# Performance work log

Measured on AMD Instinct MI355X. Metric: run time of the kernel, lower is better.

## Reference

```python
import jax, jax.numpy as jnp
import numpy as np

IN_F = 256
OUT_F = 256
ALPHA = 0.2  # leaky-relu slope
NEG_INF = -9e15


def setup_inputs() -> dict:
    key = jax.random.key(0)
    ks = jax.random.split(key, 8)
    N_e, N_kc = 10000, 2000
    exercise_h = jax.random.normal(ks[0], (N_e, IN_F), dtype=jnp.float32)
    kc_h = jax.random.normal(ks[1], (N_kc, IN_F), dtype=jnp.float32)
    adj = jax.random.randint(ks[2], (N_e, N_kc), 0, 2, dtype=jnp.int32)
    # parameters (kaiming-ish scaling)
    W1 = jax.random.normal(ks[3], (IN_F, OUT_F), dtype=jnp.float32) * np.sqrt(2.0 / IN_F)
    E = jax.random.normal(ks[4], (IN_F, OUT_F), dtype=jnp.float32) * np.sqrt(2.0 / IN_F)
    a = jax.random.normal(ks[5], (2 * OUT_F, 1), dtype=jnp.float32) * np.sqrt(2.0 / (2 * OUT_F))
    rd_w = jax.random.normal(ks[6], (OUT_F, 2 * OUT_F), dtype=jnp.float32) * np.sqrt(2.0 / (2 * OUT_F))
    rd_b = jnp.zeros((OUT_F,), dtype=jnp.float32)
    return {"exercise_h": exercise_h, "kc_h": kc_h, "adj": adj,
            "W1": W1, "E": E, "a": a, "rd_w": rd_w, "rd_b": rd_b}


def reference(exercise_h, kc_h, adj, W1, E, a, rd_w, rd_b):
    kc_Wh = kc_h @ W1            # [N_kc, D]
    ex_Wh = exercise_h @ W1      # [N_e, D]
    # a . concat(ex_Wh_i, kc_Wh_j) == a1.ex_Wh_i + a2.kc_Wh_j  (avoids [N_e,N_kc,2D] tensor)
    a1 = a[:OUT_F, 0]
    a2 = a[OUT_F:, 0]
    e = jax.nn.leaky_relu((ex_Wh @ a1)[:, None] + (kc_Wh @ a2)[None, :], negative_slope=ALPHA)  # [N_e, N_kc]
    logits = jnp.where(adj > 0, e, jnp.float32(NEG_INF))
    attention = jax.nn.softmax(logits, axis=1)
    new_kc = attention @ kc_Wh           # [N_e, D]
    ex_Eh = exercise_h @ E               # [N_e, D]
    feat = jnp.concatenate([new_kc, new_kc * ex_Eh], axis=1)  # [N_e, 2D]
    out = feat @ rd_w.T + rd_b
    return jax.nn.elu(out)
```

## Files before the change

### kernel.cpp

```cpp
#include <hip/hip_runtime.h>

#define N_E 10000
#define N_KC 2000
#define KPAD 2048
#define ALPHA 0.2f

typedef __attribute__((ext_vector_type(8))) short short8;
typedef __attribute__((ext_vector_type(4))) float f32x4;

__device__ float g_w1a1[256];
__device__ float g_w1a2[256];
__device__ float g_s[N_E];
__device__ float g_t[KPAD];
__device__ __align__(16) unsigned short g_kc_bf[N_KC * 256];
__device__ __align__(16) unsigned short g_exh_pk[625 * 8 * 512];
__device__ __align__(16) unsigned short g_W1T_pk[16 * 8 * 512];
__device__ __align__(16) unsigned short g_ET_pk[16 * 8 * 512];
__device__ __align__(16) unsigned short g_rdw_pk[16 * 16 * 512];
__device__ __align__(16) unsigned short g_kcWh_pk[16 * 64 * 512];

__device__ __forceinline__ unsigned short f2bf(float f) {
  union { float f; unsigned int u; } v; v.f = f;
  unsigned int r = v.u + 0x7FFFu + ((v.u >> 16) & 1u);
  return (unsigned short)(r >> 16);
}

__device__ __forceinline__ void cvt_store4(float4 v, unsigned short* dst) {
  ushort4 o;
  o.x = f2bf(v.x); o.y = f2bf(v.y); o.z = f2bf(v.z); o.w = f2bf(v.w);
  *reinterpret_cast<ushort4*>(dst) = o;
}

__global__ __launch_bounds__(256) void prep_kernel(
    const float* __restrict__ exh, const float* __restrict__ kc_h,
    const float* __restrict__ W1, const float* __restrict__ E,
    const float* __restrict__ a, const float* __restrict__ rd_w) {
  int b = blockIdx.x, tid = threadIdx.x;
  if (b < 625) {
#pragma unroll
    for (int s2 = 0; s2 < 2; ++s2) {
      int sId = tid + s2 * 256;
      int kt = sId >> 6, lane = sId & 63;
      int g = lane >> 4, r = lane & 15;
      const float* src = exh + (size_t)(b * 16 + r) * 256 + kt * 32 + g * 8;
      unsigned short* dst = g_exh_pk + ((size_t)b * 8 + kt) * 512 + lane * 8;
      cvt_store4(*(const float4*)src, dst);
      cvt_store4(*(const float4*)(src + 4), dst + 4);
    }
  } else if (b < 750) {
    for (int q = 0; q < 4; ++q) {
      int idx = (b - 625) * 1024 + q * 256 + tid;
      cvt_store4(((const float4*)kc_h)[idx], g_kc_bf + (size_t)idx * 4);
    }
  } else if (b < 782) {
#pragma unroll
    for (int s2 = 0; s2 < 2; ++s2) {
      int sId = (b - 750) * 512 + tid + s2 * 256;
      int ct = sId >> 10, rem = sId & 1023;
      int kt = rem >> 6, lane = rem & 63;
      int g = lane >> 4, r = lane & 15;
      const float* src = rd_w + (size_t)(ct * 16 + r) * 512 + kt * 32 + g * 8;
      unsigned short* dst = g_rdw_pk + (size_t)sId * 8;
      cvt_store4(*(const float4*)src, dst);
      cvt_store4(*(const float4*)(src + 4), dst + 4);
    }
  } else if (b < 798) {
#pragma unroll
    for (int s2 = 0; s2 < 2; ++s2) {
      int sId = (b - 782) * 512 + tid + s2 * 256;
      int ct = sId >> 9, rem = sId & 511;
      int kt = rem >> 6, lane = rem & 63;
      int g = lane >> 4, r = lane & 15;
      int col = ct * 16 + r, k = kt * 32 + g * 8;
      unsigned short* dst = g_W1T_pk + (size_t)sId * 8;
      ushort4 o0, o1;
      o0.x = f2bf(W1[(k + 0) * 256 + col]); o0.y = f2bf(W1[(k + 1) * 256 + col]);
      o0.z = f2bf(W1[(k + 2) * 256 + col]); o0.w = f2bf(W1[(k + 3) * 256 + col]);
      o1.x = f2bf(W1[(k + 4) * 256 + col]); o1.y = f2bf(W1[(k + 5) * 256 + col]);
      o1.z = f2bf(W1[(k + 6) * 256 + col]); o1.w = f2bf(W1[(k + 7) * 256 + col]);
      *(ushort4*)dst = o0; *(ushort4*)(dst + 4) = o1;
    }
  } else if (b < 814) {
#pragma unroll
    for (int s2 = 0; s2 < 2; ++s2) {
      int sId = (b - 798) * 512 + tid + s2 * 256;
      int ct = sId >> 9, rem = sId & 511;
      int kt = rem >> 6, lane = rem & 63;
      int g = lane >> 4, r = lane & 15;
      int col = ct * 16 + r, k = kt * 32 + g * 8;
      unsigned short* dst = g_ET_pk + (size_t)sId * 8;
      ushort4 o0, o1;
      o0.x = f2bf(E[(k + 0) * 256 + col]); o0.y = f2bf(E[(k + 1) * 256 + col]);
      o0.z = f2bf(E[(k + 2) * 256 + col]); o0.w = f2bf(E[(k + 3) * 256 + col]);
      o1.x = f2bf(E[(k + 4) * 256 + col]); o1.y = f2bf(E[(k + 5) * 256 + col]);
      o1.z = f2bf(E[(k + 6) * 256 + col]); o1.w = f2bf(E[(k + 7) * 256 + col]);
      *(ushort4*)dst = o0; *(ushort4*)(dst + 4) = o1;
    }
  } else if (b < 816) {
    const float* av = a + (b - 814) * 256;
    float acc = 0.f;
    for (int q = 0; q < 64; ++q) {
      float4 wv = *(const float4*)(W1 + (size_t)tid * 256 + q * 4);
      float4 a4 = *(const float4*)(av + q * 4);
      acc += wv.x * a4.x + wv.y * a4.y + wv.z * a4.z + wv.w * a4.w;
    }
    if (b == 814) g_w1a1[tid] = acc; else g_w1a2[tid] = acc;
  } else {
    for (int idx = tid; idx < 16 * 2 * 512; idx += 256) {
      int ct = idx >> 10, rem = idx & 1023;
      int kt = 62 + (rem >> 9), off = rem & 511;
      g_kcWh_pk[((size_t)ct * 64 + kt) * 512 + off] = 0;
    }
    if (tid < 48) g_t[2000 + tid] = 0.f;
  }
}

__global__ __launch_bounds__(256) void st_kernel(
    const float* __restrict__ exh, const float* __restrict__ kc_h) {
  int tid = threadIdx.x, lane = tid & 63, w = tid >> 6;
  int row = blockIdx.x * 4 + w;
  bool is_s = row < N_E;
  const float* src = is_s ? (exh + (size_t)row * 256)
                          : (kc_h + (size_t)(row - N_E) * 256);
  const float* wv = is_s ? g_w1a1 : g_w1a2;
  float4 x = *(const float4*)(src + lane * 4);
  float4 c = *(const float4*)(wv + lane * 4);
  float d = x.x * c.x + x.y * c.y + x.z * c.z + x.w * c.w;
  for (int off = 32; off; off >>= 1) d += __shfl_down(d, off, 64);
  if (lane == 0) { if (is_s) g_s[row] = d; else g_t[row - N_E] = d; }
}

__global__ __launch_bounds__(256) void kc_mfma_kernel() {
  int tid = threadIdx.x, lane = tid & 63, w = tid >> 6;
  int r = lane & 15, g = lane >> 4;
  int j0 = blockIdx.x * 16;
  f32x4 acc[4] = {{0.f,0.f,0.f,0.f},{0.f,0.f,0.f,0.f},
                  {0.f,0.f,0.f,0.f},{0.f,0.f,0.f,0.f}};
  for (int kk = 0; kk < 8; ++kk) {
    int k = kk * 32 + g * 8;
    short8 afrag = *(const short8*)(g_kc_bf + (size_t)(j0 + r) * 256 + k);
#pragma unroll
    for (int n = 0; n < 4; ++n) {
      short8 bfrag =
          *(const short8*)(g_W1T_pk + ((size_t)(w * 4 + n) * 8 + kk) * 512 +
                           lane * 8);
      acc[n] = __builtin_amdgcn_mfma_f32_16x16x32_bf16(afrag, bfrag, acc[n],
                                                       0, 0, 0);
    }
  }
  int j = j0 + g * 4;
  int kt = j >> 5, lsub = ((j >> 3) & 3) * 16 + r, sub = (g & 1) * 4;
#pragma unroll
  for (int n = 0; n < 4; ++n) {
    int ct = w * 4 + n;
    ushort4 o;
    o.x = f2bf(acc[n][0]); o.y = f2bf(acc[n][1]);
    o.z = f2bf(acc[n][2]); o.w = f2bf(acc[n][3]);
    *reinterpret_cast<ushort4*>(
        g_kcWh_pk + ((size_t)ct * 64 + kt) * 512 + lsub * 8 + sub) = o;
  }
}

#define PST 280
#define FST 536
__global__ __launch_bounds__(512) void main_kernel(
    const int* __restrict__ adj, const float* __restrict__ rd_b,
    float* __restrict__ out) {
  __shared__ float t_s[KPAD];
  __shared__ __align__(16) unsigned short p_s[2][16 * PST];
  __shared__ __align__(16) unsigned short feat_s[16 * FST];
  __shared__ float ds_part[8][16];
  __shared__ float dtot[16];

  int tid = threadIdx.x;
  int w = tid >> 6, lane = tid & 63;
  int r = lane & 15, g = lane >> 4;
  int i0 = blockIdx.x * 16;
  int c0e = w * 32;

  for (int q = tid; q < KPAD / 4; q += 512)
    ((float4*)t_s)[q] = ((const float4*)g_t)[q];
  float sv = g_s[i0 + r];
  const int* arow = adj + (size_t)(i0 + r) * N_KC;
  __syncthreads();

  f32x4 accP[2] = {{0.f,0.f,0.f,0.f},{0.f,0.f,0.f,0.f}};
  float dsum = 0.f;

  auto gen = [&](int c) {
    int kk = c * 8 + w;
    unsigned short* dst = &p_s[c & 1][r * PST + w * 32 + g * 8];
    int c0 = kk * 32 + g * 8;
    int4 pk = {0, 0, 0, 0};
    if (kk < 63 && c0 < N_KC) {
      int4 a0 = *(const int4*)(arow + c0);
      int4 a1 = *(const int4*)(arow + c0 + 4);
      float4 t0 = *(const float4*)(t_s + c0);
      float4 t1 = *(const float4*)(t_s + c0 + 4);
      float tv[8] = {t0.x, t0.y, t0.z, t0.w, t1.x, t1.y, t1.z, t1.w};
      int av[8] = {a0.x, a0.y, a0.z, a0.w, a1.x, a1.y, a1.z, a1.w};
      unsigned int ub[8];
#pragma unroll
      for (int j = 0; j < 8; ++j) {
        float x = sv + tv[j];
        float lx = fmaxf(x, ALPHA * x);
        float pv = (av[j] > 0) ? __expf(lx) : 0.f;
        dsum += pv;
        ub[j] = __float_as_uint(pv) + 0x8000u;
      }
      pk.x = (int)((ub[0] >> 16) | (ub[1] & 0xFFFF0000u));
      pk.y = (int)((ub[2] >> 16) | (ub[3] & 0xFFFF0000u));
      pk.z = (int)((ub[4] >> 16) | (ub[5] & 0xFFFF0000u));
      pk.w = (int)((ub[6] >> 16) | (ub[7] & 0xFFFF0000u));
    }
    *(int4*)dst = pk;
  };

  auto mfma_chunk = [&](int c) {
#pragma unroll
    for (int u = 0; u < 8; ++u) {
      int kk = c * 8 + u;
      short8 af = *(const short8*)&p_s[c & 1][r * PST + u * 32 + g * 8];
#pragma unroll
      for (int n = 0; n < 2; ++n) {
        short8 bf = *(const short8*)(g_kcWh_pk +
                                     ((size_t)(w * 2 + n) * 64 + kk) * 512 +
                                     lane * 8);
        accP[n] = __builtin_amdgcn_mfma_f32_16x16x32_bf16(af, bf, accP[n],
                                                          0, 0, 0);
      }
    }
  };

  gen(0);
  __syncthreads();
  for (int c = 1; c < 8; ++c) {
    gen(c);
    mfma_chunk(c - 1);
    __syncthreads();
  }
  mfma_chunk(7);

  dsum += __shfl_xor(dsum, 16, 64);
  dsum += __shfl_xor(dsum, 32, 64);
  if (lane < 16) ds_part[w][lane] = dsum;

  f32x4 accE[2] = {{0.f,0.f,0.f,0.f},{0.f,0.f,0.f,0.f}};
#pragma unroll
  for (int kk = 0; kk < 8; ++kk) {
    short8 af = *(const short8*)(g_exh_pk +
                                 ((size_t)blockIdx.x * 8 + kk) * 512 + lane * 8);
#pragma unroll
    for (int n = 0; n < 2; ++n) {
      short8 bf = *(const short8*)(g_ET_pk +
                                   ((size_t)(w * 2 + n) * 8 + kk) * 512 +
                                   lane * 8);
      accE[n] = __builtin_amdgcn_mfma_f32_16x16x32_bf16(af, bf, accE[n],
                                                        0, 0, 0);
    }
  }
  __syncthreads();
  if (tid < 16) {
    float s = 0.f;
#pragma unroll
    for (int ww = 0; ww < 8; ++ww) s += ds_part[ww][tid];
    dtot[tid] = 1.f / fmaxf(s, 1e-30f);
  }
  __syncthreads();

#pragma unroll
  for (int n = 0; n < 2; ++n) {
    int col = c0e + n * 16 + r;
#pragma unroll
    for (int q = 0; q < 4; ++q) {
      int row = g * 4 + q;
      float nk = accP[n][q] * dtot[row];
      feat_s[row * FST + col] = f2bf(nk);
      feat_s[row * FST + 256 + col] = f2bf(nk * accE[n][q]);
    }
  }
  __syncthreads();

  f32x4 accO[2] = {{0.f,0.f,0.f,0.f},{0.f,0.f,0.f,0.f}};
#pragma unroll
  for (int kk = 0; kk < 16; ++kk) {
    int k = kk * 32 + g * 8;
    short8 af = *(const short8*)&feat_s[r * FST + k];
#pragma unroll
    for (int n = 0; n < 2; ++n) {
      short8 bf = *(const short8*)(g_rdw_pk +
                                   ((size_t)(w * 2 + n) * 16 + kk) * 512 +
                                   lane * 8);
      accO[n] = __builtin_amdgcn_mfma_f32_16x16x32_bf16(af, bf, accO[n],
                                                        0, 0, 0);
    }
  }
#pragma unroll
  for (int n = 0; n < 2; ++n) {
    int col = c0e + n * 16 + r;
    float bias = rd_b[col];
#pragma unroll
    for (int q = 0; q < 4; ++q) {
      int row = g * 4 + q;
      float x = accO[n][q] + bias;
      float res = x > 0.f ? x : (__expf(x) - 1.f);
      out[(size_t)(i0 + row) * 256 + col] = res;
    }
  }
}

extern "C" void kernel_launch(void* const* d_in, const int* in_sizes, int n_in,
                              void* d_out, int out_size, void* d_ws,
                              size_t ws_size, hipStream_t stream) {
  const float* exh  = (const float*)d_in[0];
  const float* kc_h = (const float*)d_in[1];
  const int*   adj  = (const int*)d_in[2];
  const float* W1   = (const float*)d_in[3];
  const float* E    = (const float*)d_in[4];
  const float* a    = (const float*)d_in[5];
  const float* rd_w = (const float*)d_in[6];
  const float* rd_b = (const float*)d_in[7];
  float* out = (float*)d_out;

  prep_kernel<<<817, 256, 0, stream>>>(exh, kc_h, W1, E, a, rd_w);
  st_kernel<<<(N_E + N_KC) / 4, 256, 0, stream>>>(exh, kc_h);
  kc_mfma_kernel<<<N_KC / 16, 256, 0, stream>>>();
  main_kernel<<<N_E / 16, 512, 0, stream>>>(adj, rd_b, out);
}
```

Measured before the change: 199.4 us.

## Pack adjacency into bitmask and fuse score and bf16 staging into consumers

A prep kernel now compresses the int32 adjacency matrix into a per-row bitmask, so the main kernel reads compact mask words from shared memory instead of streaming adj while it builds the softmax tiles. The separate score kernel and the bf16 staging buffers for exercise_h and kc_h are removed. The kc-side scores are folded into the kc MFMA epilogue, and the exercise-side scores plus the bf16 packing are computed in the main kernel's prologue. The P@V MFMA loop also gets register double-buffering of its fragments, and the main kernel gets an occupancy hint. The full adj read still happens in the prep pass, so the gain depends on that pass streaming adj more efficiently and on saving a launch and the intermediate traffic.

```diff
diff --git a/kernel.cpp b/kernel.cpp
--- a/kernel.cpp
+++ b/kernel.cpp
@@ -9,11 +9,8 @@
 typedef __attribute__((ext_vector_type(4))) float f32x4;
 
 __device__ float g_w1a1[256];
-__device__ float g_w1a2[256];
-__device__ float g_s[N_E];
 __device__ float g_t[KPAD];
-__device__ __align__(16) unsigned short g_kc_bf[N_KC * 256];
-__device__ __align__(16) unsigned short g_exh_pk[625 * 8 * 512];
+__device__ unsigned g_bm[N_E * 64];
 __device__ __align__(16) unsigned short g_W1T_pk[16 * 8 * 512];
 __device__ __align__(16) unsigned short g_ET_pk[16 * 8 * 512];
 __device__ __align__(16) unsigned short g_rdw_pk[16 * 16 * 512];
@@ -31,31 +28,28 @@
   *reinterpret_cast<ushort4*>(dst) = o;
 }
 
-__global__ __launch_bounds__(256) void prep_kernel(
-    const float* __restrict__ exh, const float* __restrict__ kc_h,
-    const float* __restrict__ W1, const float* __restrict__ E,
-    const float* __restrict__ a, const float* __restrict__ rd_w) {
+__global__ __launch_bounds__(256) void prep_pack_kernel(
+    const int* __restrict__ adj, const float* __restrict__ W1,
+    const float* __restrict__ E, const float* __restrict__ a,
+    const float* __restrict__ rd_w) {
   int b = blockIdx.x, tid = threadIdx.x;
-  if (b < 625) {
+  if (b < 2500) {
+    int id = b * 256 + tid;
+    int row = id >> 6, wd = id & 63;
+    const int* p = adj + (size_t)row * 2000 + wd * 32;
+    unsigned m = 0;
+    int nq = (wd < 62) ? 8 : ((wd == 62) ? 4 : 0);
+    for (int q = 0; q < nq; ++q) {
+      int4 v = *(const int4*)(p + q * 4);
+      unsigned mm = (v.x > 0 ? 1u : 0u) | (v.y > 0 ? 2u : 0u) |
+                    (v.z > 0 ? 4u : 0u) | (v.w > 0 ? 8u : 0u);
+      m |= mm << (q * 4);
+    }
+    g_bm[(size_t)row * 64 + wd] = m;
+  } else if (b < 2532) {
 #pragma unroll
     for (int s2 = 0; s2 < 2; ++s2) {
-      int sId = tid + s2 * 256;
-      int kt = sId >> 6, lane = sId & 63;
-      int g = lane >> 4, r = lane & 15;
-      const float* src = exh + (size_t)(b * 16 + r) * 256 + kt * 32 + g * 8;
-      unsigned short* dst = g_exh_pk + ((size_t)b * 8 + kt) * 512 + lane * 8;
-      cvt_store4(*(const float4*)src, dst);
-      cvt_store4(*(const float4*)(src + 4), dst + 4);
-    }
-  } else if (b < 750) {
-    for (int q = 0; q < 4; ++q) {
-      int idx = (b - 625) * 1024 + q * 256 + tid;
-      cvt_store4(((const float4*)kc_h)[idx], g_kc_bf + (size_t)idx * 4);
-    }
-  } else if (b < 782) {
-#pragma unroll
-    for (int s2 = 0; s2 < 2; ++s2) {
-      int sId = (b - 750) * 512 + tid + s2 * 256;
+      int sId = (b - 2500) * 512 + tid + s2 * 256;
       int ct = sId >> 10, rem = sId & 1023;
       int kt = rem >> 6, lane = rem & 63;
       int g = lane >> 4, r = lane & 15;
@@ -64,10 +58,10 @@
       cvt_store4(*(const float4*)src, dst);
       cvt_store4(*(const float4*)(src + 4), dst + 4);
     }
-  } else if (b < 798) {
+  } else if (b < 2548) {
 #pragma unroll
     for (int s2 = 0; s2 < 2; ++s2) {
-      int sId = (b - 782) * 512 + tid + s2 * 256;
+      int sId = (b - 2532) * 512 + tid + s2 * 256;
       int ct = sId >> 9, rem = sId & 511;
       int kt = rem >> 6, lane = rem & 63;
       int g = lane >> 4, r = lane & 15;
@@ -80,10 +74,10 @@
       o1.z = f2bf(W1[(k + 6) * 256 + col]); o1.w = f2bf(W1[(k + 7) * 256 + col]);
       *(ushort4*)dst = o0; *(ushort4*)(dst + 4) = o1;
     }
-  } else if (b < 814) {
+  } else if (b < 2564) {
 #pragma unroll
     for (int s2 = 0; s2 < 2; ++s2) {
-      int sId = (b - 798) * 512 + tid + s2 * 256;
+      int sId = (b - 2548) * 512 + tid + s2 * 256;
       int ct = sId >> 9, rem = sId & 511;
       int kt = rem >> 6, lane = rem & 63;
       int g = lane >> 4, r = lane & 15;
@@ -96,15 +90,14 @@
       o1.z = f2bf(E[(k + 6) * 256 + col]); o1.w = f2bf(E[(k + 7) * 256 + col]);
       *(ushort4*)dst = o0; *(ushort4*)(dst + 4) = o1;
     }
-  } else if (b < 816) {
-    const float* av = a + (b - 814) * 256;
+  } else if (b == 2564) {
     float acc = 0.f;
     for (int q = 0; q < 64; ++q) {
       float4 wv = *(const float4*)(W1 + (size_t)tid * 256 + q * 4);
-      float4 a4 = *(const float4*)(av + q * 4);
+      float4 a4 = *(const float4*)(a + q * 4);
       acc += wv.x * a4.x + wv.y * a4.y + wv.z * a4.z + wv.w * a4.w;
     }
-    if (b == 814) g_w1a1[tid] = acc; else g_w1a2[tid] = acc;
+    g_w1a1[tid] = acc;
   } else {
     for (int idx = tid; idx < 16 * 2 * 512; idx += 256) {
       int ct = idx >> 10, rem = idx & 1023;
@@ -115,22 +108,9 @@
   }
 }
 
-__global__ __launch_bounds__(256) void st_kernel(
-    const float* __restrict__ exh, const float* __restrict__ kc_h) {
-  int tid = threadIdx.x, lane = tid & 63, w = tid >> 6;
-  int row = blockIdx.x * 4 + w;
-  bool is_s = row < N_E;
-  const float* src = is_s ? (exh + (size_t)row * 256)
-                          : (kc_h + (size_t)(row - N_E) * 256);
-  const float* wv = is_s ? g_w1a1 : g_w1a2;
-  float4 x = *(const float4*)(src + lane * 4);
-  float4 c = *(const float4*)(wv + lane * 4);
-  float d = x.x * c.x + x.y * c.y + x.z * c.z + x.w * c.w;
-  for (int off = 32; off; off >>= 1) d += __shfl_down(d, off, 64);
-  if (lane == 0) { if (is_s) g_s[row] = d; else g_t[row - N_E] = d; }
-}
-
-__global__ __launch_bounds__(256) void kc_mfma_kernel() {
+__global__ __launch_bounds__(256) void kc_mfma_kernel(
+    const float* __restrict__ kc_h, const float* __restrict__ a) {
+  __shared__ float tred[4][4][4];
   int tid = threadIdx.x, lane = tid & 63, w = tid >> 6;
   int r = lane & 15, g = lane >> 4;
   int j0 = blockIdx.x * 16;
@@ -138,14 +118,16 @@
                   {0.f,0.f,0.f,0.f},{0.f,0.f,0.f,0.f}};
   for (int kk = 0; kk < 8; ++kk) {
     int k = kk * 32 + g * 8;
-    short8 afrag = *(const short8*)(g_kc_bf + (size_t)(j0 + r) * 256 + k);
+    const float* src = kc_h + (size_t)(j0 + r) * 256 + k;
+    float4 x0 = *(const float4*)src, x1 = *(const float4*)(src + 4);
+    short8 af = {(short)f2bf(x0.x), (short)f2bf(x0.y), (short)f2bf(x0.z),
+                 (short)f2bf(x0.w), (short)f2bf(x1.x), (short)f2bf(x1.y),
+                 (short)f2bf(x1.z), (short)f2bf(x1.w)};
 #pragma unroll
     for (int n = 0; n < 4; ++n) {
-      short8 bfrag =
-          *(const short8*)(g_W1T_pk + ((size_t)(w * 4 + n) * 8 + kk) * 512 +
-                           lane * 8);
-      acc[n] = __builtin_amdgcn_mfma_f32_16x16x32_bf16(afrag, bfrag, acc[n],
-                                                       0, 0, 0);
+      short8 bf = *(const short8*)(g_W1T_pk + ((size_t)(w * 4 + n) * 8 + kk) *
+                                                  512 + lane * 8);
+      acc[n] = __builtin_amdgcn_mfma_f32_16x16x32_bf16(af, bf, acc[n], 0, 0, 0);
     }
   }
   int j = j0 + g * 4;
@@ -159,52 +141,93 @@
     *reinterpret_cast<ushort4*>(
         g_kcWh_pk + ((size_t)ct * 64 + kt) * 512 + lsub * 8 + sub) = o;
   }
+  float a2v[4];
+#pragma unroll
+  for (int n = 0; n < 4; ++n) a2v[n] = a[256 + w * 64 + n * 16 + r];
+  float tp[4];
+#pragma unroll
+  for (int q = 0; q < 4; ++q)
+    tp[q] = acc[0][q] * a2v[0] + acc[1][q] * a2v[1] + acc[2][q] * a2v[2] +
+            acc[3][q] * a2v[3];
+#pragma unroll
+  for (int off = 1; off < 16; off <<= 1)
+#pragma unroll
+    for (int q = 0; q < 4; ++q) tp[q] += __shfl_xor(tp[q], off, 64);
+  if (r == 0)
+#pragma unroll
+    for (int q = 0; q < 4; ++q) tred[w][g][q] = tp[q];
+  __syncthreads();
+  if (tid < 16)
+    g_t[j0 + tid] = tred[0][tid >> 2][tid & 3] + tred[1][tid >> 2][tid & 3] +
+                    tred[2][tid >> 2][tid & 3] + tred[3][tid >> 2][tid & 3];
 }
 
 #define PST 280
 #define FST 536
-__global__ __launch_bounds__(512) void main_kernel(
-    const int* __restrict__ adj, const float* __restrict__ rd_b,
+#define BMST 65
+__global__ __launch_bounds__(512, 6) void main_kernel(
+    const float* __restrict__ exh, const float* __restrict__ rd_b,
     float* __restrict__ out) {
   __shared__ float t_s[KPAD];
+  __shared__ unsigned bm_s[16 * BMST];
   __shared__ __align__(16) unsigned short p_s[2][16 * PST];
   __shared__ __align__(16) unsigned short feat_s[16 * FST];
   __shared__ float ds_part[8][16];
-  __shared__ float dtot[16];
+  __shared__ float red16[16];
 
   int tid = threadIdx.x;
   int w = tid >> 6, lane = tid & 63;
   int r = lane & 15, g = lane >> 4;
   int i0 = blockIdx.x * 16;
-  int c0e = w * 32;
+  unsigned short* exh_pk_s = feat_s;
 
   for (int q = tid; q < KPAD / 4; q += 512)
     ((float4*)t_s)[q] = ((const float4*)g_t)[q];
-  float sv = g_s[i0 + r];
-  const int* arow = adj + (size_t)(i0 + r) * N_KC;
-  __syncthreads();
+  for (int q = tid; q < 16 * 64; q += 512) {
+    int rr = q >> 6, wd = q & 63;
+    bm_s[rr * BMST + wd] = g_bm[(size_t)(i0 + rr) * 64 + wd];
+  }
+  {
+    const float* xsrc = exh + (size_t)(i0 + r) * 256 + w * 32 + g * 8;
+    float4 x0 = *(const float4*)xsrc, x1 = *(const float4*)(xsrc + 4);
+    unsigned short* dst = exh_pk_s + w * 512 + lane * 8;
+    cvt_store4(x0, dst); cvt_store4(x1, dst + 4);
+    const float* wsrc = g_w1a1 + w * 32 + g * 8;
+    float4 w0 = *(const float4*)wsrc, w1 = *(const float4*)(wsrc + 4);
+    float sp = x0.x * w0.x + x0.y * w0.y + x0.z * w0.z + x0.w * w0.w +
+               x1.x * w1.x + x1.y * w1.y + x1.z * w1.z + x1.w * w1.w;
+    sp += __shfl_xor(sp, 16, 64);
+    sp += __shfl_xor(sp, 32, 64);
+    if (lane < 16) ds_part[w][lane] = sp;
+  }
+  __syncthreads();
+  if (tid < 16) {
+    float sv = 0.f;
+#pragma unroll
+    for (int ww = 0; ww < 8; ++ww) sv += ds_part[ww][tid];
+    red16[tid] = sv;
+  }
+  __syncthreads();
+  float sv = red16[r];
 
   f32x4 accP[2] = {{0.f,0.f,0.f,0.f},{0.f,0.f,0.f,0.f}};
   float dsum = 0.f;
 
   auto gen = [&](int c) {
     int kk = c * 8 + w;
-    unsigned short* dst = &p_s[c & 1][r * PST + w * 32 + g * 8];
-    int c0 = kk * 32 + g * 8;
     int4 pk = {0, 0, 0, 0};
-    if (kk < 63 && c0 < N_KC) {
-      int4 a0 = *(const int4*)(arow + c0);
-      int4 a1 = *(const int4*)(arow + c0 + 4);
+    if (kk < 63) {
+      int c0 = kk * 32 + g * 8;
+      unsigned mb = (bm_s[r * BMST + kk] >> (g * 8)) & 0xFFu;
       float4 t0 = *(const float4*)(t_s + c0);
       float4 t1 = *(const float4*)(t_s + c0 + 4);
       float tv[8] = {t0.x, t0.y, t0.z, t0.w, t1.x, t1.y, t1.z, t1.w};
-      int av[8] = {a0.x, a0.y, a0.z, a0.w, a1.x, a1.y, a1.z, a1.w};
-      unsigned int ub[8];
+      unsigned ub[8];
 #pragma unroll
       for (int j = 0; j < 8; ++j) {
         float x = sv + tv[j];
         float lx = fmaxf(x, ALPHA * x);
-        float pv = (av[j] > 0) ? __expf(lx) : 0.f;
+        float pv = ((mb >> j) & 1u) ? __expf(lx) : 0.f;
         dsum += pv;
         ub[j] = __float_as_uint(pv) + 0x8000u;
       }
@@ -213,22 +236,29 @@
       pk.z = (int)((ub[4] >> 16) | (ub[5] & 0xFFFF0000u));
       pk.w = (int)((ub[6] >> 16) | (ub[7] & 0xFFFF0000u));
     }
-    *(int4*)dst = pk;
+    *(int4*)&p_s[c & 1][r * PST + w * 32 + g * 8] = pk;
   };
 
   auto mfma_chunk = [&](int c) {
+    const unsigned short* pb = p_s[c & 1];
+    const unsigned short* bb0 =
+        g_kcWh_pk + ((size_t)(w * 2 + 0) * 64 + c * 8) * 512 + lane * 8;
+    const unsigned short* bb1 =
+        g_kcWh_pk + ((size_t)(w * 2 + 1) * 64 + c * 8) * 512 + lane * 8;
+    short8 af = *(const short8*)&pb[r * PST + g * 8];
+    short8 b0 = *(const short8*)bb0;
+    short8 b1 = *(const short8*)bb1;
 #pragma unroll
     for (int u = 0; u < 8; ++u) {
-      int kk = c * 8 + u;
-      short8 af = *(const short8*)&p_s[c & 1][r * PST + u * 32 + g * 8];
-#pragma unroll
-      for (int n = 0; n < 2; ++n) {
-        short8 bf = *(const short8*)(g_kcWh_pk +
-                                     ((size_t)(w * 2 + n) * 64 + kk) * 512 +
-                                     lane * 8);
-        accP[n] = __builtin_amdgcn_mfma_f32_16x16x32_bf16(af, bf, accP[n],
-                                                          0, 0, 0);
+      short8 naf = af, nb0 = b0, nb1 = b1;
+      if (u < 7) {
+        naf = *(const short8*)&pb[r * PST + (u + 1) * 32 + g * 8];
+        nb0 = *(const short8*)(bb0 + (u + 1) * 512);
+        nb1 = *(const short8*)(bb1 + (u + 1) * 512);
       }
+      accP[0] = __builtin_amdgcn_mfma_f32_16x16x32_bf16(af, b0, accP[0], 0, 0, 0);
+      accP[1] = __builtin_amdgcn_mfma_f32_16x16x32_bf16(af, b1, accP[1], 0, 0, 0);
+      af = naf; b0 = nb0; b1 = nb1;
     }
   };
 
@@ -248,15 +278,12 @@
   f32x4 accE[2] = {{0.f,0.f,0.f,0.f},{0.f,0.f,0.f,0.f}};
 #pragma unroll
   for (int kk = 0; kk < 8; ++kk) {
-    short8 af = *(const short8*)(g_exh_pk +
-                                 ((size_t)blockIdx.x * 8 + kk) * 512 + lane * 8);
+    short8 af = *(const short8*)(exh_pk_s + kk * 512 + lane * 8);
 #pragma unroll
     for (int n = 0; n < 2; ++n) {
-      short8 bf = *(const short8*)(g_ET_pk +
-                                   ((size_t)(w * 2 + n) * 8 + kk) * 512 +
-                                   lane * 8);
-      accE[n] = __builtin_amdgcn_mfma_f32_16x16x32_bf16(af, bf, accE[n],
-                                                        0, 0, 0);
+      short8 bf = *(const short8*)(g_ET_pk + ((size_t)(w * 2 + n) * 8 + kk) *
+                                                 512 + lane * 8);
+      accE[n] = __builtin_amdgcn_mfma_f32_16x16x32_bf16(af, bf, accE[n], 0, 0, 0);
     }
   }
   __syncthreads();
@@ -264,17 +291,18 @@
     float s = 0.f;
 #pragma unroll
     for (int ww = 0; ww < 8; ++ww) s += ds_part[ww][tid];
-    dtot[tid] = 1.f / fmaxf(s, 1e-30f);
-  }
-  __syncthreads();
-
+    red16[tid] = 1.f / fmaxf(s, 1e-30f);
+  }
+  __syncthreads();
+
+  int c0e = w * 32;
 #pragma unroll
   for (int n = 0; n < 2; ++n) {
     int col = c0e + n * 16 + r;
 #pragma unroll
     for (int q = 0; q < 4; ++q) {
       int row = g * 4 + q;
-      float nk = accP[n][q] * dtot[row];
+      float nk = accP[n][q] * red16[row];
       feat_s[row * FST + col] = f2bf(nk);
       feat_s[row * FST + 256 + col] = f2bf(nk * accE[n][q]);
     }
@@ -288,11 +316,9 @@
     short8 af = *(const short8*)&feat_s[r * FST + k];
 #pragma unroll
     for (int n = 0; n < 2; ++n) {
-      short8 bf = *(const short8*)(g_rdw_pk +
-                                   ((size_t)(w * 2 + n) * 16 + kk) * 512 +
-                                   lane * 8);
-      accO[n] = __builtin_amdgcn_mfma_f32_16x16x32_bf16(af, bf, accO[n],
-                                                        0, 0, 0);
+      short8 bf = *(const short8*)(g_rdw_pk + ((size_t)(w * 2 + n) * 16 + kk) *
+                                                  512 + lane * 8);
+      accO[n] = __builtin_amdgcn_mfma_f32_16x16x32_bf16(af, bf, accO[n], 0, 0, 0);
     }
   }
 #pragma unroll
@@ -322,8 +348,7 @@
   const float* rd_b = (const float*)d_in[7];
   float* out = (float*)d_out;
 
-  prep_kernel<<<817, 256, 0, stream>>>(exh, kc_h, W1, E, a, rd_w);
-  st_kernel<<<(N_E + N_KC) / 4, 256, 0, stream>>>(exh, kc_h);
-  kc_mfma_kernel<<<N_KC / 16, 256, 0, stream>>>();
-  main_kernel<<<N_E / 16, 512, 0, stream>>>(adj, rd_b, out);
-}
+  prep_pack_kernel<<<2566, 256, 0, stream>>>(adj, W1, E, a, rd_w);
+  kc_mfma_kernel<<<N_KC / 16, 256, 0, stream>>>(kc_h, a);
+  main_kernel<<<N_E / 16, 512, 0, stream>>>(exh, rd_b, out);
+}
```

Result: slower. 232.4 us (+16.6%).
